# Optimization experiments

Hardware: AMD Instinct MI355X
Metric: run time of the kernel (lower is better)

## Reference

```python
import jax, jax.numpy as jnp
import numpy as np

QLEN, MLEN, CMLEN, BSZ, D_MODEL = 1024, 1024, 512, 2, 1024
N_HEAD, D_HEAD, D_INNER = 16, 64, 4096
KLEN = MLEN + CMLEN + QLEN
LN_EPS = 1e-5


def _layer_norm(x, scale, bias):
    mu = jnp.mean(x, axis=-1, keepdims=True)
    var = jnp.var(x, axis=-1, keepdims=True)
    return (x - mu) * jax.lax.rsqrt(var + LN_EPS) * scale + bias


def _rel_shift(x):
    # x: [qlen, klen, bsz, n_head]  (Transformer-XL relative shift)
    q, k, b, n = x.shape
    x = jnp.concatenate([jnp.zeros((q, 1, b, n), x.dtype), x], axis=1)
    x = x.reshape(k + 1, q, b, n)[1:]
    return x.reshape(q, k, b, n)


def setup_inputs() -> dict:
    key = jax.random.key(0)
    ks = jax.random.split(key, 10)
    s = 0.02
    # causal mask: query i (absolute pos MLEN_TOT+i) cannot attend to key j > MLEN_TOT+i
    mlen_tot = KLEN - QLEN
    i = jnp.arange(QLEN)[:, None]
    j = jnp.arange(KLEN)[None, :]
    attn_mask = j > (i + mlen_tot)
    return {
        "input_ids": jax.random.normal(ks[0], (QLEN, BSZ, D_MODEL), jnp.float32),
        "pos_emb": jax.random.normal(ks[1], (KLEN, D_MODEL), jnp.float32),
        "mem": jax.random.normal(ks[2], (MLEN, BSZ, D_MODEL), jnp.float32),
        "c_mem": jax.random.normal(ks[3], (CMLEN, BSZ, D_MODEL), jnp.float32),
        "attn_mask": attn_mask,
        "qkv_w": jax.random.normal(ks[4], (D_MODEL, 3 * N_HEAD * D_HEAD), jnp.float32) * s,
        "r_w": jax.random.normal(ks[5], (D_MODEL, N_HEAD * D_HEAD), jnp.float32) * s,
        "o_w": jax.random.normal(ks[6], (N_HEAD * D_HEAD, D_MODEL), jnp.float32) * s,
        "r_w_bias": jax.random.normal(ks[7], (N_HEAD, D_HEAD), jnp.float32) * s,
        "r_r_bias": jax.random.normal(ks[8], (N_HEAD, D_HEAD), jnp.float32) * s,
        "ln_attn_scale": jnp.ones((D_MODEL,), jnp.float32),
        "ln_attn_bias": jnp.zeros((D_MODEL,), jnp.float32),
        "ff_w1": jax.random.normal(ks[9], (D_MODEL, D_INNER), jnp.float32) * s,
        "ff_b1": jnp.zeros((D_INNER,), jnp.float32),
        "ff_w2": jax.random.normal(jax.random.fold_in(key, 11), (D_INNER, D_MODEL), jnp.float32) * s,
        "ff_b2": jnp.zeros((D_MODEL,), jnp.float32),
        "ln_ff_scale": jnp.ones((D_MODEL,), jnp.float32),
        "ln_ff_bias": jnp.zeros((D_MODEL,), jnp.float32),
    }


def reference(input_ids, pos_emb, mem, c_mem, attn_mask, qkv_w, r_w, o_w,
              r_w_bias, r_r_bias, ln_attn_scale, ln_attn_bias,
              ff_w1, ff_b1, ff_w2, ff_b2, ln_ff_scale, ln_ff_bias):
    qlen, bsz, d_model = input_ids.shape
    n_head, d_head = r_w_bias.shape
    scale = 1.0 / np.sqrt(d_head)

    # _concat_memories + cat with current sequence (seq-first, dim 0)
    mems = jnp.concatenate([mem, c_mem], axis=0)
    cat = jnp.concatenate([mems, input_ids], axis=0)          # [klen, b, d]

    w_heads = cat @ qkv_w                                     # [klen, b, 3*h*dh]
    w_q, w_k, w_v = jnp.split(w_heads, 3, axis=-1)
    w_q = w_q[-qlen:]
    klen = w_k.shape[0]

    w_q = w_q.reshape(qlen, bsz, n_head, d_head)
    w_k = w_k.reshape(klen, bsz, n_head, d_head)
    w_v = w_v.reshape(klen, bsz, n_head, d_head)
    r_k = (pos_emb @ r_w).reshape(klen, n_head, d_head)       # [klen, h, dh]

    AC = jnp.einsum('ibnd,jbnd->ijbn', w_q + r_w_bias, w_k)
    BD = jnp.einsum('ibnd,jnd->ijbn', w_q + r_r_bias, r_k)
    BD = _rel_shift(BD)
    attn_score = (AC + BD) * scale                            # [q, k, b, h]

    attn_score = jnp.where(attn_mask[:, :, None, None], jnp.float32(-1e30), attn_score)
    attn_prob = jax.nn.softmax(attn_score, axis=1)

    attn_vec = jnp.einsum('ijbn,jbnd->ibnd', attn_prob, w_v)
    attn_vec = attn_vec.reshape(qlen, bsz, n_head * d_head)
    attn_out = attn_vec @ o_w

    # post-lnorm residual (pre_lnorm=False)
    attn_res = _layer_norm(input_ids + attn_out, ln_attn_scale, ln_attn_bias)

    # PositionwiseFF (post-lnorm)
    h = jax.nn.relu(attn_res @ ff_w1 + ff_b1) @ ff_w2 + ff_b2
    out = _layer_norm(attn_res + h, ln_ff_scale, ln_ff_bias)
    return out
```

## Files before the change

### kernel.cpp

```cpp
#include <hip/hip_runtime.h>
#include <hip/hip_bf16.h>

#define QLEN 1024
#define KLEN 2560
#define MTOT 1536
#define BSZ 2
#define NH 16
#define DH 64
#define DMODEL 1024
#define DINNER 4096

typedef short bf16x8 __attribute__((ext_vector_type(8)));
typedef float f32x4  __attribute__((ext_vector_type(4)));

__device__ __forceinline__ short f2bf(float f) {
    union { float f; unsigned u; } v; v.f = f;
    unsigned r = v.u + 0x7FFFu + ((v.u >> 16) & 1u);
    return (short)(r >> 16);
}
__device__ __forceinline__ float bf2f(short s) {
    union { unsigned u; float f; } v; v.u = ((unsigned)(unsigned short)s) << 16;
    return v.f;
}
__device__ __forceinline__ unsigned pack2(float a, float b) {
    return (unsigned)(unsigned short)f2bf(a) | ((unsigned)(unsigned short)f2bf(b) << 16);
}

#define GLOAD16(g, l)                                                        \
    __builtin_amdgcn_global_load_lds(                                        \
        (const __attribute__((address_space(1))) unsigned int*)(g),          \
        (__attribute__((address_space(3))) unsigned int*)(l), 16, 0, 0)

__device__ __forceinline__ void tr_body(
    const float* __restrict__ in, short* __restrict__ out,
    int K, int N, int bx, int by, int tid, float (*ts)[65])
{
    const int k0 = by * 64, n0 = bx * 64;
    const int r = tid >> 2, cb = (tid & 3) * 16;
    #pragma unroll
    for (int u = 0; u < 16; u += 4) {
        const float4 v = *(const float4*)(in + (size_t)(k0 + r) * N + n0 + cb + u);
        ts[r][cb + u] = v.x; ts[r][cb + u + 1] = v.y;
        ts[r][cb + u + 2] = v.z; ts[r][cb + u + 3] = v.w;
    }
    __syncthreads();
    #pragma unroll
    for (int p = 0; p < 4; p++) {
        const int wr_ = (tid >> 4) + p * 16;
        const int c   = (tid & 15) * 4;
        uint2 pk;
        pk.x = pack2(ts[c][wr_], ts[c + 1][wr_]);
        pk.y = pack2(ts[c + 2][wr_], ts[c + 3][wr_]);
        *(uint2*)(out + (size_t)(n0 + wr_) * K + k0 + c) = pk;
    }
}

__global__ __launch_bounds__(256) void prep_all(
    const float* __restrict__ mem, const float* __restrict__ cmem,
    const float* __restrict__ inp, short* __restrict__ catb,
    const float* __restrict__ pos, short* __restrict__ posb,
    const float* __restrict__ qkv_w, short* __restrict__ qkv_wt,
    const float* __restrict__ r_w, short* __restrict__ r_wt,
    const float* __restrict__ o_w, short* __restrict__ o_wt,
    const float* __restrict__ ff_w1, short* __restrict__ ff1t,
    const float* __restrict__ ff_w2, short* __restrict__ ff2t)
{
    __shared__ float ts[64][65];
    const int bid = blockIdx.x;
    const int tid = threadIdx.x;
    if (bid < 2560) {
        const int i = bid * 256 + tid;
        const int row = i >> 7, c = (i & 127) * 8;
        const float* src;
        if (row < 2048)      src = mem  + (size_t)row * 1024;
        else if (row < 3072) src = cmem + (size_t)(row - 2048) * 1024;
        else                 src = inp  + (size_t)(row - 3072) * 1024;
        const float4 a = *(const float4*)(src + c);
        const float4 b = *(const float4*)(src + c + 4);
        uint4 o;
        o.x = pack2(a.x, a.y); o.y = pack2(a.z, a.w);
        o.z = pack2(b.x, b.y); o.w = pack2(b.z, b.w);
        *(uint4*)(catb + (size_t)i * 8) = o;
    } else if (bid < 3840) {
        const int i = (bid - 2560) * 256 + tid;
        const float4 a = *(const float4*)(pos + (size_t)i * 8);
        const float4 b = *(const float4*)(pos + (size_t)i * 8 + 4);
        uint4 o;
        o.x = pack2(a.x, a.y); o.y = pack2(a.z, a.w);
        o.z = pack2(b.x, b.y); o.w = pack2(b.z, b.w);
        *(uint4*)(posb + (size_t)i * 8) = o;
    } else if (bid < 4608) {
        const int r = bid - 3840; tr_body(qkv_w, qkv_wt, 1024, 3072, r % 48, r / 48, tid, ts);
    } else if (bid < 4864) {
        const int r = bid - 4608; tr_body(r_w, r_wt, 1024, 1024, r % 16, r / 16, tid, ts);
    } else if (bid < 5120) {
        const int r = bid - 4864; tr_body(o_w, o_wt, 1024, 1024, r % 16, r / 16, tid, ts);
    } else if (bid < 6144) {
        const int r = bid - 5120; tr_body(ff_w1, ff1t, 1024, 4096, r % 64, r / 64, tid, ts);
    } else {
        const int r = bid - 6144; tr_body(ff_w2, ff2t, 4096, 1024, r % 16, r / 16, tid, ts);
    }
}

__global__ __launch_bounds__(256) void vt_conv(
    const short* __restrict__ wh, short* __restrict__ vt)
{
    __shared__ short Ts[64][72];
    const int j0 = blockIdx.x * 64;
    const int bn = blockIdx.y;
    const int b = bn >> 4, n = bn & 15;
    const int tid = threadIdx.x;
    {
        const int key = tid >> 2, c = (tid & 3) * 16;
        const short* p = wh + ((size_t)(j0 + key) * BSZ + b) * 3072 + 2048 + n * 64 + c;
        *(bf16x8*)&Ts[key][c]     = *(const bf16x8*)p;
        *(bf16x8*)&Ts[key][c + 8] = *(const bf16x8*)(p + 8);
    }
    __syncthreads();
    {
        const int d = tid >> 2, kc = (tid & 3) * 16;
        __attribute__((aligned(16))) short tmp[16];
        #pragma unroll
        for (int u = 0; u < 16; u++) tmp[u] = Ts[kc + u][d];
        short* q = vt + ((size_t)(bn * 64) + d) * KLEN + j0 + kc;
        *(uint4*)q       = *(uint4*)tmp;
        *(uint4*)(q + 8) = *((uint4*)tmp + 1);
    }
}

__device__ __forceinline__ void gemm_core(
    const short* __restrict__ A, const short* __restrict__ Bt,
    short* As, short* Bs, int Kfull, int klen, int bm, int bn,
    int tid, f32x4 acc[4][4])
{
    const int w  = tid >> 6;
    const int l  = tid & 63;
    const int lg = l >> 4, lc = l & 15;
    const int wr = w >> 1, wc = w & 1;
    const int srow = 2 * w * 16 + (l >> 2);
    const int scol = (l & 3) * 8;
    const size_t aoff0 = (size_t)(bm + srow) * Kfull + scol;
    const size_t boff0 = (size_t)(bn + srow) * Kfull + scol;
    const size_t rstep = (size_t)16 * Kfull;
    short* lA0 = As + 2 * w * 512;
    short* lA1 = As + (2 * w + 1) * 512;
    short* lB0 = Bs + 2 * w * 512;
    short* lB1 = Bs + (2 * w + 1) * 512;

    for (int k0 = 0; k0 < klen; k0 += 32) {
        GLOAD16(A + aoff0 + k0, lA0);
        GLOAD16(A + aoff0 + rstep + k0, lA1);
        GLOAD16(Bt + boff0 + k0, lB0);
        GLOAD16(Bt + boff0 + rstep + k0, lB1);
        __syncthreads();
        bf16x8 af[4], bfr[4];
        #pragma unroll
        for (int m = 0; m < 4; m++)
            af[m] = *(const bf16x8*)(As + (wr * 64 + m * 16 + lc) * 32 + lg * 8);
        #pragma unroll
        for (int n = 0; n < 4; n++)
            bfr[n] = *(const bf16x8*)(Bs + (wc * 64 + n * 16 + lc) * 32 + lg * 8);
        #pragma unroll
        for (int m = 0; m < 4; m++)
            #pragma unroll
            for (int n = 0; n < 4; n++)
                acc[m][n] = __builtin_amdgcn_mfma_f32_16x16x32_bf16(
                    af[m], bfr[n], acc[m][n], 0, 0, 0);
        __syncthreads();
    }
}

__global__ __launch_bounds__(256) void gemm_g12(
    const short* __restrict__ catb, const short* __restrict__ qkv_wt,
    short* __restrict__ whb,
    const short* __restrict__ posb, const short* __restrict__ r_wt,
    short* __restrict__ rkb)
{
    __shared__ short As[4096], Bs[4096];
    const int tid = threadIdx.x;
    int id = blockIdx.x;
    const short *A, *Bt; short* Cb; int N, bm, bn;
    if (id < 960) { A = catb; Bt = qkv_wt; Cb = whb; N = 3072;
                    bm = (id / 24) * 128; bn = (id % 24) * 128; }
    else { id -= 960; A = posb; Bt = r_wt; Cb = rkb; N = 1024;
           bm = (id / 8) * 128; bn = (id % 8) * 128; }

    f32x4 acc[4][4];
    #pragma unroll
    for (int m = 0; m < 4; m++)
        #pragma unroll
        for (int n = 0; n < 4; n++) acc[m][n] = (f32x4){0.f, 0.f, 0.f, 0.f};
    gemm_core(A, Bt, As, Bs, 1024, 1024, bm, bn, tid, acc);

    const int w = tid >> 6, l = tid & 63, lg = l >> 4, lc = l & 15;
    const int wr = w >> 1, wc = w & 1;
    #pragma unroll
    for (int m = 0; m < 4; m++)
        #pragma unroll
        for (int n = 0; n < 4; n++) {
            const int col = bn + wc * 64 + n * 16 + lc;
            #pragma unroll
            for (int r = 0; r < 4; r++) {
                const int row = bm + wr * 64 + m * 16 + lg * 4 + r;
                Cb[(size_t)row * N + col] = f2bf(acc[m][n][r]);
            }
        }
}

__global__ __launch_bounds__(256) void gemm_relu(
    const short* __restrict__ A, const short* __restrict__ Bt,
    const float* __restrict__ bias, short* __restrict__ Cb,
    int N, int K)
{
    __shared__ short As[4096], Bs[4096];
    const int tid = threadIdx.x;
    const int bm = blockIdx.y * 128, bn = blockIdx.x * 128;
    f32x4 acc[4][4];
    #pragma unroll
    for (int m = 0; m < 4; m++)
        #pragma unroll
        for (int n = 0; n < 4; n++) acc[m][n] = (f32x4){0.f, 0.f, 0.f, 0.f};
    gemm_core(A, Bt, As, Bs, K, K, bm, bn, tid, acc);

    const int w = tid >> 6, l = tid & 63, lg = l >> 4, lc = l & 15;
    const int wr = w >> 1, wc = w & 1;
    #pragma unroll
    for (int m = 0; m < 4; m++)
        #pragma unroll
        for (int n = 0; n < 4; n++) {
            const int col = bn + wc * 64 + n * 16 + lc;
            const float bv = bias[col];
            #pragma unroll
            for (int r = 0; r < 4; r++) {
                const int row = bm + wr * 64 + m * 16 + lg * 4 + r;
                Cb[(size_t)row * N + col] = f2bf(fmaxf(acc[m][n][r] + bv, 0.0f));
            }
        }
}

__global__ __launch_bounds__(256) void gemm_split(
    const short* __restrict__ A, const short* __restrict__ Bt,
    float* __restrict__ C0, float* __restrict__ C1,
    int N, int Kfull, int Ksub)
{
    __shared__ short As[4096], Bs[4096];
    const int tid = threadIdx.x;
    const int z = blockIdx.z;
    const int bm = blockIdx.y * 128, bn = blockIdx.x * 128;
    float* C = z ? C1 : C0;
    f32x4 acc[4][4];
    #pragma unroll
    for (int m = 0; m < 4; m++)
        #pragma unroll
        for (int n = 0; n < 4; n++) acc[m][n] = (f32x4){0.f, 0.f, 0.f, 0.f};
    gemm_core(A + z * Ksub, Bt + z * Ksub, As, Bs, Kfull, Ksub, bm, bn, tid, acc);

    const int w = tid >> 6, l = tid & 63, lg = l >> 4, lc = l & 15;
    const int wr = w >> 1, wc = w & 1;
    #pragma unroll
    for (int m = 0; m < 4; m++)
        #pragma unroll
        for (int n = 0; n < 4; n++) {
            const int col = bn + wc * 64 + n * 16 + lc;
            #pragma unroll
            for (int r = 0; r < 4; r++) {
                const int row = bm + wr * 64 + m * 16 + lg * 4 + r;
                C[(size_t)row * N + col] = acc[m][n][r];
            }
        }
}

__global__ __launch_bounds__(512, 2) void attn_mfma(
    const short* __restrict__ wh,
    const short* __restrict__ vt,
    const short* __restrict__ rk,
    const float* __restrict__ rwb,
    const float* __restrict__ rrb,
    short* __restrict__ po,
    float* __restrict__ ml)
{
    __shared__ __align__(16) short Ks[64 * 64];
    __shared__ __align__(16) short Vs[64 * 64];
    __shared__ __align__(16) short Rs[192 * 64];
    __shared__ __align__(16) short Ps[8][16 * 64];

    const int bid = blockIdx.x;
    const int ibp = (bid >> 3) & 7;
    const int z   = (bid >> 6) & 1;
    const int bn  = ((bid & 7) << 2) | (bid >> 7);
    const int i0  = ibp * 128;
    const int b   = bn >> 4, n = bn & 15;
    const int tid = threadIdx.x;
    const int w   = tid >> 6;
    const int l   = tid & 63;
    const int lg  = l >> 4;
    const int lc  = l & 15;
    const int i_base = i0 + 16 * w;

    bf16x8 aqw[2], aqr[2];
    {
        const int i = i_base + lc;
        const short* qp = wh + ((size_t)(MTOT + i) * BSZ + b) * 3072 + n * 64;
        #pragma unroll
        for (int kc = 0; kc < 2; kc++) {
            const bf16x8 q8 = *(const bf16x8*)(qp + kc * 32 + lg * 8);
            const int d0 = kc * 32 + lg * 8;
            #pragma unroll
            for (int e = 0; e < 8; e++) {
                const float qv = bf2f(q8[e]);
                aqw[kc][e] = f2bf(qv + rwb[n * 64 + d0 + e]);
                aqr[kc][e] = f2bf(qv + rrb[n * 64 + d0 + e]);
            }
        }
    }

    f32x4 o_acc[4];
    #pragma unroll
    for (int nt = 0; nt < 4; nt++) o_acc[nt] = (f32x4){0.f, 0.f, 0.f, 0.f};
    float mrun[4]  = {0.f, 0.f, 0.f, 0.f};
    float lpart[4] = {0.f, 0.f, 0.f, 0.f};

    const int jend   = i0 + 1664;
    const int jhalf  = i0 / 2 + 832;
    const int jstart = z ? jhalf : 0;
    const int jstop  = z ? jend  : jhalf;

    const int kr = tid >> 3, kc = tid & 7;
    const size_t whK = (size_t)b * 3072 + 1024 + n * 64;
    const size_t vtK = (size_t)(bn * 64) * KLEN;

    bf16x8 pk, pv;
    pk = *(const bf16x8*)(wh + (size_t)(jstart + kr) * (BSZ * 3072) + whK + kc * 8);
    pv = *(const bf16x8*)(vt + vtK + (size_t)kr * KLEN + jstart + kc * 8);

    for (int j0 = jstart; j0 < jstop; j0 += 64) {
        __syncthreads();
        bf16x8 rreg[3];
        const int mbase = j0 - i0 + 896;
        #pragma unroll
        for (int u = 0; u < 3; u++) {
            const int m = mbase + kr + 64 * u;
            rreg[u] = (m < KLEN)
                ? *(const bf16x8*)(rk + (size_t)m * 1024 + n * 64 + kc * 8)
                : (bf16x8){0, 0, 0, 0, 0, 0, 0, 0};
        }
        *(bf16x8*)(Ks + kr * 64 + ((kc ^ (kr & 7)) * 8)) = pk;
        *(bf16x8*)(Vs + kr * 64 + ((kc ^ (kr & 7)) * 8)) = pv;
        #pragma unroll
        for (int u = 0; u < 3; u++) {
            const int row = kr + 64 * u;
            *(bf16x8*)(Rs + row * 64 + ((kc ^ (row & 7)) * 8)) = rreg[u];
        }
        const int jn = j0 + 64;
        if (jn < jstop) {
            pk = *(const bf16x8*)(wh + (size_t)(jn + kr) * (BSZ * 3072) + whK + kc * 8);
            pv = *(const bf16x8*)(vt + vtK + (size_t)kr * KLEN + jn + kc * 8);
        }
        __syncthreads();

        __builtin_amdgcn_s_setprio(1);
        f32x4 sfr[4];
        #pragma unroll
        for (int jt = 0; jt < 4; jt++) {
            const int row = 16 * jt + lc;
            const int c0 = (lg ^ (row & 7)) * 8, c1 = ((4 + lg) ^ (row & 7)) * 8;
            const bf16x8 bk0 = *(const bf16x8*)(Ks + row * 64 + c0);
            const bf16x8 bk1 = *(const bf16x8*)(Ks + row * 64 + c1);
            f32x4 acc = (f32x4){0.f, 0.f, 0.f, 0.f};
            acc = __builtin_amdgcn_mfma_f32_16x16x32_bf16(aqw[0], bk0, acc, 0, 0, 0);
            acc = __builtin_amdgcn_mfma_f32_16x16x32_bf16(aqw[1], bk1, acc, 0, 0, 0);
            sfr[jt] = acc;
        }
        f32x4 dr[5];
        #pragma unroll
        for (int mt = 0; mt < 5; mt++) {
            const int rrow = 16 * mt + lc + 112 - 16 * w;
            const int c0 = (lg ^ (rrow & 7)) * 8, c1 = ((4 + lg) ^ (rrow & 7)) * 8;
            const bf16x8 br0 = *(const bf16x8*)(Rs + rrow * 64 + c0);
            const bf16x8 br1 = *(const bf16x8*)(Rs + rrow * 64 + c1);
            f32x4 acc = (f32x4){0.f, 0.f, 0.f, 0.f};
            acc = __builtin_amdgcn_mfma_f32_16x16x32_bf16(aqr[0], br0, acc, 0, 0, 0);
            acc = __builtin_amdgcn_mfma_f32_16x16x32_bf16(aqr[1], br1, acc, 0, 0, 0);
            dr[mt] = acc;
        }
        __builtin_amdgcn_s_setprio(0);

        #pragma unroll
        for (int r = 0; r < 4; r++) {
            const int q   = 4 * lg + r;
            const int o   = lc + 15 - q;
            const int src = (l & 48) | (o & 15);
            float sv[4];
            float mx = -1e30f;
            #pragma unroll
            for (int jt = 0; jt < 4; jt++) {
                const float v0 = __shfl(dr[jt][r], src);
                const float v1 = __shfl(dr[jt + 1][r], src);
                const float bd = (o < 16) ? v0 : v1;
                float s = (sfr[jt][r] + bd) * 0.125f;
                if (z) {
                    const int j = j0 + 16 * jt + lc;
                    if (j > i_base + q + MTOT) s = -1e30f;
                }
                sv[jt] = s;
                mx = fmaxf(mx, s);
            }
            if (__any(mx - mrun[r] > 8.0f)) {
                #pragma unroll
                for (int msk = 1; msk <= 8; msk <<= 1)
                    mx = fmaxf(mx, __shfl_xor(mx, msk));
                const float mnew = fmaxf(mrun[r], mx);
                const float corr = __expf(mrun[r] - mnew);
                mrun[r] = mnew;
                lpart[r] *= corr;
                #pragma unroll
                for (int nt = 0; nt < 4; nt++) o_acc[nt][r] *= corr;
            }
            float ps = 0.f;
            #pragma unroll
            for (int jt = 0; jt < 4; jt++) {
                const float p = __expf(sv[jt] - mrun[r]);
                ps += p;
                Ps[w][q * 64 + (((2 * jt + (lc >> 3)) ^ (q & 7)) * 8) + (lc & 7)] = f2bf(p);
            }
            lpart[r] += ps;
        }

        asm volatile("s_waitcnt lgkmcnt(0)" ::: "memory");
        __builtin_amdgcn_sched_barrier(0);

        __builtin_amdgcn_s_setprio(1);
        const int pc0 = (lg ^ (lc & 7)) * 8, pc1 = ((4 + lg) ^ (lc & 7)) * 8;
        const bf16x8 pa0 = *(const bf16x8*)(Ps[w] + lc * 64 + pc0);
        const bf16x8 pa1 = *(const bf16x8*)(Ps[w] + lc * 64 + pc1);
        #pragma unroll
        for (int nt = 0; nt < 4; nt++) {
            const int row = 16 * nt + lc;
            const int c0 = (lg ^ (row & 7)) * 8, c1 = ((4 + lg) ^ (row & 7)) * 8;
            const bf16x8 bv0 = *(const bf16x8*)(Vs + row * 64 + c0);
            const bf16x8 bv1 = *(const bf16x8*)(Vs + row * 64 + c1);
            o_acc[nt] = __builtin_amdgcn_mfma_f32_16x16x32_bf16(pa0, bv0, o_acc[nt], 0, 0, 0);
            o_acc[nt] = __builtin_amdgcn_mfma_f32_16x16x32_bf16(pa1, bv1, o_acc[nt], 0, 0, 0);
        }
        __builtin_amdgcn_s_setprio(0);
    }

    const size_t blk = (size_t)z * 256 + ibp * 32 + bn;
    #pragma unroll
    for (int r = 0; r < 4; r++) {
        float lr = lpart[r];
        #pragma unroll
        for (int msk = 1; msk <= 8; msk <<= 1)
            lr += __shfl_xor(lr, msk);
        const int q = 16 * w + 4 * lg + r;
        #pragma unroll
        for (int nt = 0; nt < 4; nt++)
            po[(blk * 128 + q) * 64 + 16 * nt + lc] = f2bf(o_acc[nt][r]);
        if (lc == 0) {
            ml[(blk * 128 + q) * 2 + 0] = mrun[r];
            ml[(blk * 128 + q) * 2 + 1] = lr;
        }
    }
}

__global__ __launch_bounds__(256) void attn_merge(
    const short* __restrict__ po, const float* __restrict__ ml,
    short* __restrict__ av)
{
    const int blk = blockIdx.x;
    const int ib2 = blk >> 5, bn = blk & 31;
    const int b = bn >> 4, n = bn & 15;
    const int tid = threadIdx.x;
    const int q64 = tid >> 2, dc = (tid & 3) * 16;
    const int i = ib2 * 64 + q64;
    const size_t r0 = ((size_t)(i >> 7) * 32 + bn) * 128 + (i & 127);
    const size_t r1 = ((size_t)(256 + (i >> 7) * 32 + bn)) * 128 + (i & 127);
    const float m0 = ml[r0 * 2], l0 = ml[r0 * 2 + 1];
    const float m1 = ml[r1 * 2], l1 = ml[r1 * 2 + 1];
    const float M = fmaxf(m0, m1);
    const float c0 = __expf(m0 - M), c1 = __expf(m1 - M);
    const float invL = 1.0f / (l0 * c0 + l1 * c1);
    const bf16x8 a0 = *(const bf16x8*)(po + r0 * 64 + dc);
    const bf16x8 a1 = *(const bf16x8*)(po + r0 * 64 + dc + 8);
    const bf16x8 b0 = *(const bf16x8*)(po + r1 * 64 + dc);
    const bf16x8 b1 = *(const bf16x8*)(po + r1 * 64 + dc + 8);
    __attribute__((aligned(16))) short ov[16];
    #pragma unroll
    for (int e = 0; e < 8; e++) {
        ov[e]     = f2bf((bf2f(a0[e]) * c0 + bf2f(b0[e]) * c1) * invL);
        ov[e + 8] = f2bf((bf2f(a1[e]) * c0 + bf2f(b1[e]) * c1) * invL);
    }
    short* op = av + ((size_t)i * BSZ + b) * 1024 + n * 64 + dc;
    *(uint4*)op       = *(uint4*)ov;
    *(uint4*)(op + 8) = *((uint4*)ov + 1);
}

template <bool WB, bool HASB>
__global__ __launch_bounds__(256) void ln_fuse(
    const float* __restrict__ p0, const float* __restrict__ p1,
    const float* __restrict__ badd, const float* __restrict__ res,
    const float* __restrict__ scale, const float* __restrict__ bias,
    float* __restrict__ out, short* __restrict__ outb)
{
    const int row = blockIdx.x;
    const int tid = threadIdx.x;
    const size_t base = (size_t)row * 1024 + tid * 4;
    const float4 a = *(const float4*)(p0 + base);
    const float4 b = *(const float4*)(p1 + base);
    const float4 rv = *(const float4*)(res + base);
    float v[4] = {a.x + b.x + rv.x, a.y + b.y + rv.y,
                  a.z + b.z + rv.z, a.w + b.w + rv.w};
    if (HASB) {
        const float4 bb = *(const float4*)(badd + tid * 4);
        v[0] += bb.x; v[1] += bb.y; v[2] += bb.z; v[3] += bb.w;
    }
    float s  = v[0] + v[1] + v[2] + v[3];
    float ss = v[0]*v[0] + v[1]*v[1] + v[2]*v[2] + v[3]*v[3];
    #pragma unroll
    for (int off = 32; off >= 1; off >>= 1) {
        s  += __shfl_down(s, off);
        ss += __shfl_down(ss, off);
    }
    __shared__ float red[8];
    const int lane = tid & 63, wid = tid >> 6;
    if (lane == 0) { red[wid] = s; red[4 + wid] = ss; }
    __syncthreads();
    if (tid == 0) {
        red[0] = red[0] + red[1] + red[2] + red[3];
        red[4] = red[4] + red[5] + red[6] + red[7];
    }
    __syncthreads();
    const float mean = red[0] * (1.0f / 1024.0f);
    const float var  = red[4] * (1.0f / 1024.0f) - mean * mean;
    const float rstd = rsqrtf(var + 1e-5f);
    const float4 sc = *(const float4*)(scale + tid * 4);
    const float4 bi = *(const float4*)(bias + tid * 4);
    float4 o;
    o.x = (v[0] - mean) * rstd * sc.x + bi.x;
    o.y = (v[1] - mean) * rstd * sc.y + bi.y;
    o.z = (v[2] - mean) * rstd * sc.z + bi.z;
    o.w = (v[3] - mean) * rstd * sc.w + bi.w;
    *(float4*)(out + base) = o;
    if (WB) {
        uint2 pk;
        pk.x = pack2(o.x, o.y);
        pk.y = pack2(o.z, o.w);
        *(uint2*)(outb + base) = pk;
    }
}

extern "C" void kernel_launch(void* const* d_in, const int* in_sizes, int n_in,
                              void* d_out, int out_size, void* d_ws, size_t ws_size,
                              hipStream_t stream) {
    const float* input_ids = (const float*)d_in[0];
    const float* pos_emb   = (const float*)d_in[1];
    const float* mem       = (const float*)d_in[2];
    const float* c_mem     = (const float*)d_in[3];
    const float* qkv_w     = (const float*)d_in[5];
    const float* r_w       = (const float*)d_in[6];
    const float* o_w       = (const float*)d_in[7];
    const float* r_w_bias  = (const float*)d_in[8];
    const float* r_r_bias  = (const float*)d_in[9];
    const float* ln_a_s    = (const float*)d_in[10];
    const float* ln_a_b    = (const float*)d_in[11];
    const float* ff_w1     = (const float*)d_in[12];
    const float* ff_b1     = (const float*)d_in[13];
    const float* ff_w2     = (const float*)d_in[14];
    const float* ff_b2     = (const float*)d_in[15];
    const float* ln_f_s    = (const float*)d_in[16];
    const float* ln_f_b    = (const float*)d_in[17];

    char* base = (char*)d_ws;
    short* o_wt   = (short*)(base + 0);
    short* ff1t   = (short*)(base + 2097152);
    short* ff2t   = (short*)(base + 10485760);
    short* whb    = (short*)(base + 18874368);
    short* rkb    = (short*)(base + 50331648);
    short* qkv_wt = (short*)(base + 55574528);
    short* catb   = (short*)(base + 61865984);
    short* posb   = (short*)(base + 72351744);
    short* r_wt   = (short*)(base + 77594624);
    short* vtb    = (short*)(base + 55574528);
    short* po     = (short*)(base + 66060288);
    float* mlb    = (float*)(base + 74448896);
    short* avb    = (short*)(base + 74973184);
    float* hp0    = (float*)(base + 18874368);
    float* hp1    = (float*)(base + 27262976);
    float* ares   = (float*)(base + 35651584);
    short* aresb  = (short*)(base + 44040192);
    short* h1b    = (short*)(base + 48234496);

    const dim3 thr(256);

    prep_all<<<dim3(7168), thr, 0, stream>>>(
        mem, c_mem, input_ids, catb, pos_emb, posb,
        qkv_w, qkv_wt, r_w, r_wt, o_w, o_wt, ff_w1, ff1t, ff_w2, ff2t);
    gemm_g12<<<dim3(1120), thr, 0, stream>>>(catb, qkv_wt, whb, posb, r_wt, rkb);
    vt_conv<<<dim3(40, 32), thr, 0, stream>>>(whb, vtb);
    attn_mfma<<<dim3(512), dim3(512), 0, stream>>>(
        whb, vtb, rkb, r_w_bias, r_r_bias, po, mlb);
    attn_merge<<<dim3(512), thr, 0, stream>>>(po, mlb, avb);
    gemm_split<<<dim3(8, 16, 2), thr, 0, stream>>>(
        avb, o_wt, hp0, hp1, 1024, 1024, 512);
    ln_fuse<true, false><<<dim3(2048), thr, 0, stream>>>(
        hp0, hp1, nullptr, input_ids, ln_a_s, ln_a_b, ares, aresb);
    gemm_relu<<<dim3(32, 16), thr, 0, stream>>>(aresb, ff1t, ff_b1, h1b, 4096, 1024);
    gemm_split<<<dim3(8, 16, 2), thr, 0, stream>>>(
        h1b, ff2t, hp0, hp1, 1024, 4096, 2048);
    ln_fuse<false, true><<<dim3(2048), thr, 0, stream>>>(
        hp0, hp1, ff_b2, ares, ln_f_s, ln_f_b, (float*)d_out, nullptr);
}
```

Measured before the change: 290.9 us.

## Skip unused memory-row Q projection and ring-buffer positional keys in attention

The QKV GEMM no longer computes Q columns for memory rows, since only the last qlen query rows are used. This cuts the grid by a sixth of the QKV blocks. The attention kernel keeps positional-key rows in a 256-slot circular LDS buffer and loads only 64 new rows per tile instead of 192, with prefetch into registers. Probabilities are converted with a packed bf16 instruction. The costs are more LDS use, which may affect occupancy, and slot-index arithmetic.

Result: faster. 274.3 us (-5.7%).

```diff
diff --git a/kernel.cpp b/kernel.cpp
--- a/kernel.cpp
+++ b/kernel.cpp
@@ -23,7 +23,9 @@
     return v.f;
 }
 __device__ __forceinline__ unsigned pack2(float a, float b) {
-    return (unsigned)(unsigned short)f2bf(a) | ((unsigned)(unsigned short)f2bf(b) << 16);
+    unsigned pk;
+    asm("v_cvt_pk_bf16_f32 %0, %1, %2" : "=v"(pk) : "v"(a), "v"(b));
+    return pk;
 }
 
 #define GLOAD16(g, l)                                                        \
@@ -180,10 +182,18 @@
     const int tid = threadIdx.x;
     int id = blockIdx.x;
     const short *A, *Bt; short* Cb; int N, bm, bn;
-    if (id < 960) { A = catb; Bt = qkv_wt; Cb = whb; N = 3072;
-                    bm = (id / 24) * 128; bn = (id % 24) * 128; }
-    else { id -= 960; A = posb; Bt = r_wt; Cb = rkb; N = 1024;
-           bm = (id / 8) * 128; bn = (id % 8) * 128; }
+    if (id < 384) {
+        A = catb; Bt = qkv_wt; Cb = whb; N = 3072;
+        bm = (id >> 4) * 128; bn = (8 + (id & 15)) * 128;
+    } else if (id < 768) {
+        id -= 384;
+        A = catb; Bt = qkv_wt; Cb = whb; N = 3072;
+        bm = (24 + id / 24) * 128; bn = (id % 24) * 128;
+    } else {
+        id -= 768;
+        A = posb; Bt = r_wt; Cb = rkb; N = 1024;
+        bm = (id / 8) * 128; bn = (id % 8) * 128;
+    }
 
     f32x4 acc[4][4];
     #pragma unroll
@@ -281,7 +291,7 @@
 {
     __shared__ __align__(16) short Ks[64 * 64];
     __shared__ __align__(16) short Vs[64 * 64];
-    __shared__ __align__(16) short Rs[192 * 64];
+    __shared__ __align__(16) short Rs[256 * 64];
     __shared__ __align__(16) short Ps[8][16 * 64];
 
     const int bid = blockIdx.x;
@@ -302,14 +312,14 @@
         const int i = i_base + lc;
         const short* qp = wh + ((size_t)(MTOT + i) * BSZ + b) * 3072 + n * 64;
         #pragma unroll
-        for (int kc = 0; kc < 2; kc++) {
-            const bf16x8 q8 = *(const bf16x8*)(qp + kc * 32 + lg * 8);
-            const int d0 = kc * 32 + lg * 8;
+        for (int kc2 = 0; kc2 < 2; kc2++) {
+            const bf16x8 q8 = *(const bf16x8*)(qp + kc2 * 32 + lg * 8);
+            const int d0 = kc2 * 32 + lg * 8;
             #pragma unroll
             for (int e = 0; e < 8; e++) {
                 const float qv = bf2f(q8[e]);
-                aqw[kc][e] = f2bf(qv + rwb[n * 64 + d0 + e]);
-                aqr[kc][e] = f2bf(qv + rrb[n * 64 + d0 + e]);
+                aqw[kc2][e] = f2bf(qv + rwb[n * 64 + d0 + e]);
+                aqr[kc2][e] = f2bf(qv + rrb[n * 64 + d0 + e]);
             }
         }
     }
@@ -329,32 +339,45 @@
     const size_t whK = (size_t)b * 3072 + 1024 + n * 64;
     const size_t vtK = (size_t)(bn * 64) * KLEN;
 
-    bf16x8 pk, pv;
+    {
+        const int mbase0 = jstart - i0 + 896;
+        #pragma unroll
+        for (int u = 0; u < 2; u++) {
+            const int m = mbase0 + kr + 64 * u;
+            bf16x8 rv = (bf16x8){0, 0, 0, 0, 0, 0, 0, 0};
+            if (m < KLEN)
+                rv = *(const bf16x8*)(rk + (size_t)m * 1024 + n * 64 + kc * 8);
+            const int slot = m & 255;
+            *(bf16x8*)(Rs + slot * 64 + ((kc ^ (slot & 7)) * 8)) = rv;
+        }
+    }
+    bf16x8 pk, pv, pr;
     pk = *(const bf16x8*)(wh + (size_t)(jstart + kr) * (BSZ * 3072) + whK + kc * 8);
     pv = *(const bf16x8*)(vt + vtK + (size_t)kr * KLEN + jstart + kc * 8);
+    {
+        const int m = jstart - i0 + 1024 + kr;
+        pr = (m < KLEN)
+            ? *(const bf16x8*)(rk + (size_t)m * 1024 + n * 64 + kc * 8)
+            : (bf16x8){0, 0, 0, 0, 0, 0, 0, 0};
+    }
 
     for (int j0 = jstart; j0 < jstop; j0 += 64) {
+        const int mbase = j0 - i0 + 896;
         __syncthreads();
-        bf16x8 rreg[3];
-        const int mbase = j0 - i0 + 896;
-        #pragma unroll
-        for (int u = 0; u < 3; u++) {
-            const int m = mbase + kr + 64 * u;
-            rreg[u] = (m < KLEN)
-                ? *(const bf16x8*)(rk + (size_t)m * 1024 + n * 64 + kc * 8)
-                : (bf16x8){0, 0, 0, 0, 0, 0, 0, 0};
-        }
         *(bf16x8*)(Ks + kr * 64 + ((kc ^ (kr & 7)) * 8)) = pk;
         *(bf16x8*)(Vs + kr * 64 + ((kc ^ (kr & 7)) * 8)) = pv;
-        #pragma unroll
-        for (int u = 0; u < 3; u++) {
-            const int row = kr + 64 * u;
-            *(bf16x8*)(Rs + row * 64 + ((kc ^ (row & 7)) * 8)) = rreg[u];
+        {
+            const int slot = (mbase + 128 + kr) & 255;
+            *(bf16x8*)(Rs + slot * 64 + ((kc ^ (slot & 7)) * 8)) = pr;
         }
         const int jn = j0 + 64;
         if (jn < jstop) {
             pk = *(const bf16x8*)(wh + (size_t)(jn + kr) * (BSZ * 3072) + whK + kc * 8);
             pv = *(const bf16x8*)(vt + vtK + (size_t)kr * KLEN + jn + kc * 8);
+            const int m = jn - i0 + 1024 + kr;
+            pr = (m < KLEN)
+                ? *(const bf16x8*)(rk + (size_t)m * 1024 + n * 64 + kc * 8)
+                : (bf16x8){0, 0, 0, 0, 0, 0, 0, 0};
         }
         __syncthreads();
 
@@ -374,10 +397,10 @@
         f32x4 dr[5];
         #pragma unroll
         for (int mt = 0; mt < 5; mt++) {
-            const int rrow = 16 * mt + lc + 112 - 16 * w;
-            const int c0 = (lg ^ (rrow & 7)) * 8, c1 = ((4 + lg) ^ (rrow & 7)) * 8;
-            const bf16x8 br0 = *(const bf16x8*)(Rs + rrow * 64 + c0);
-            const bf16x8 br1 = *(const bf16x8*)(Rs + rrow * 64 + c1);
+            const int slot = (mbase + 16 * mt + lc + 112 - 16 * w) & 255;
+            const int c0 = (lg ^ (slot & 7)) * 8, c1 = ((4 + lg) ^ (slot & 7)) * 8;
+            const bf16x8 br0 = *(const bf16x8*)(Rs + slot * 64 + c0);
+            const bf16x8 br1 = *(const bf16x8*)(Rs + slot * 64 + c1);
             f32x4 acc = (f32x4){0.f, 0.f, 0.f, 0.f};
             acc = __builtin_amdgcn_mfma_f32_16x16x32_bf16(aqr[0], br0, acc, 0, 0, 0);
             acc = __builtin_amdgcn_mfma_f32_16x16x32_bf16(aqr[1], br1, acc, 0, 0, 0);
@@ -416,14 +439,19 @@
                 #pragma unroll
                 for (int nt = 0; nt < 4; nt++) o_acc[nt][r] *= corr;
             }
-            float ps = 0.f;
-            #pragma unroll
-            for (int jt = 0; jt < 4; jt++) {
-                const float p = __expf(sv[jt] - mrun[r]);
-                ps += p;
-                Ps[w][q * 64 + (((2 * jt + (lc >> 3)) ^ (q & 7)) * 8) + (lc & 7)] = f2bf(p);
-            }
-            lpart[r] += ps;
+            float p0 = __expf(sv[0] - mrun[r]);
+            float p1 = __expf(sv[1] - mrun[r]);
+            float p2 = __expf(sv[2] - mrun[r]);
+            float p3 = __expf(sv[3] - mrun[r]);
+            lpart[r] += (p0 + p1) + (p2 + p3);
+            const unsigned pk01 = pack2(p0, p1);
+            const unsigned pk23 = pack2(p2, p3);
+            short* pw = Ps[w] + q * 64 + (lc & 7);
+            const int qs = q & 7;
+            pw[(((0 + (lc >> 3)) ^ qs) * 8)] = (short)(pk01 & 0xffffu);
+            pw[(((2 + (lc >> 3)) ^ qs) * 8)] = (short)(pk01 >> 16);
+            pw[(((4 + (lc >> 3)) ^ qs) * 8)] = (short)(pk23 & 0xffffu);
+            pw[(((6 + (lc >> 3)) ^ qs) * 8)] = (short)(pk23 >> 16);
         }
 
         asm volatile("s_waitcnt lgkmcnt(0)" ::: "memory");
@@ -595,7 +623,7 @@
     prep_all<<<dim3(7168), thr, 0, stream>>>(
         mem, c_mem, input_ids, catb, pos_emb, posb,
         qkv_w, qkv_wt, r_w, r_wt, o_w, o_wt, ff_w1, ff1t, ff_w2, ff2t);
-    gemm_g12<<<dim3(1120), thr, 0, stream>>>(catb, qkv_wt, whb, posb, r_wt, rkb);
+    gemm_g12<<<dim3(928), thr, 0, stream>>>(catb, qkv_wt, whb, posb, r_wt, rkb);
     vt_conv<<<dim3(40, 32), thr, 0, stream>>>(whb, vtb);
     attn_mfma<<<dim3(512), dim3(512), 0, stream>>>(
         whb, vtb, rkb, r_w_bias, r_r_bias, po, mlb);
```
